# Kernel tuning notes

Measured on AMD Instinct MI355X. Metric: run time of the kernel, lower is better.

Reference implementation:

```python
import jax, jax.numpy as jnp
import numpy as np

N = 50000      # total nodes
E = 800000     # total edges
B = 512        # number of graphs (batch size)
D_IN, H, D_OUT = 5, 96, 192
EPS = 1e-5


def setup_inputs() -> dict:
    key = jax.random.key(0)
    ks = jax.random.split(key, 20)
    s = lambda d: 1.0 / np.sqrt(d)
    inp = {
        "x": jax.random.normal(ks[0], (N, D_IN), jnp.float32),
        "edge_index": jax.random.randint(ks[1], (2, E), 0, N, jnp.int64),
        "batch": jnp.sort(jax.random.randint(ks[2], (N,), 0, B, jnp.int64)),
        "W_in": jax.random.normal(ks[3], (D_IN, H), jnp.float32) * s(D_IN),
        "b_in": jnp.zeros((H,), jnp.float32),
        "W1": jax.random.normal(ks[4], (H, H), jnp.float32) * s(H),
        "b1": jnp.zeros((H,), jnp.float32),
        "g1": jnp.ones((H,), jnp.float32),
        "be1": jnp.zeros((H,), jnp.float32),
        "W2": jax.random.normal(ks[5], (H, H), jnp.float32) * s(H),
        "b2": jnp.zeros((H,), jnp.float32),
        "g2": jnp.ones((H,), jnp.float32),
        "be2": jnp.zeros((H,), jnp.float32),
        "W_out": jax.random.normal(ks[6], (H, D_OUT), jnp.float32) * s(H),
        "b_out": jnp.zeros((D_OUT,), jnp.float32),
        "ln_g": jnp.ones((D_OUT,), jnp.float32),
        "ln_b": jnp.zeros((D_OUT,), jnp.float32),
    }
    return inp


def gcn_conv(h, W, b, src, dst):
    # PyG GCNConv: h' = D^{-1/2} (A + I) D^{-1/2} (h W) + b, deg from self-looped graph
    h = h @ W                                           # [N, H]
    deg = jnp.ones((N,), h.dtype).at[dst].add(jnp.ones((E,), h.dtype))
    dinv = jax.lax.rsqrt(deg)                           # [N]
    coef = dinv[src] * dinv[dst]                        # [E]
    agg = jnp.zeros_like(h).at[dst].add(h[src] * coef[:, None])
    agg = agg + h * (dinv * dinv)[:, None]              # self-loop term
    return agg + b


def batch_norm(x, g, b):
    m = x.mean(0)
    v = x.var(0)
    return g * (x - m) * jax.lax.rsqrt(v + EPS) + b


def reference(x, edge_index, batch, W_in, b_in, W1, b1, g1, be1, W2, b2, g2, be2,
              W_out, b_out, ln_g, ln_b):
    src, dst = edge_index[0], edge_index[1]
    h = jax.nn.relu(x @ W_in + b_in)
    for (W, bb, g, be) in ((W1, b1, g1, be1), (W2, b2, g2, be2)):
        r = h
        h = gcn_conv(h, W, bb, src, dst)
        h = jax.nn.relu(batch_norm(h, g, be))           # dropout = identity (eval)
        h = h + r
    counts = jnp.zeros((B,), h.dtype).at[batch].add(1.0)
    pooled = jax.ops.segment_sum(h, batch, num_segments=B)
    pooled = pooled / jnp.maximum(counts, 1.0)[:, None]  # global_mean_pool [B, H]
    out = pooled @ W_out + b_out                         # [B, D_OUT]
    mu = out.mean(-1, keepdims=True)
    var = out.var(-1, keepdims=True)
    return ln_g * (out - mu) * jax.lax.rsqrt(var + EPS) + ln_b
```

## Files before the change

### kernel.cpp

```cpp
#include <hip/hip_runtime.h>
#include <hip/hip_bf16.h>
#include <stdint.h>

#define NN 50000
#define EE 800000
#define BB 512
#define HH 96
#define DIN 5
#define DOUT 192
#define EPSV 1e-5f
#define NBANK 32
#define HWS 48
#define NB_GATHER 3125
#define NBUK 512
#define BUKN 98
#define FILLB 128
#define FCHUNK (EE / FILLB)

__device__ inline float blo(uint32_t w) { return __uint_as_float(w << 16); }
__device__ inline float bhi(uint32_t w) { return __uint_as_float(w & 0xffff0000u); }
__device__ inline uint32_t packbf(float a, float b) {
    uint32_t ua = __float_as_uint(a); ua += 0x7fffu + ((ua >> 16) & 1u);
    uint32_t ub = __float_as_uint(b); ub += 0x7fffu + ((ub >> 16) & 1u);
    return (ua >> 16) | (ub & 0xffff0000u);
}

__global__ __launch_bounds__(256) void k_bhist(const int* __restrict__ dst,
                                               int* __restrict__ histgb) {
    __shared__ int hist[NBUK];
    int tid = threadIdx.x;
    for (int j = tid; j < NBUK; j += 256) hist[j] = 0;
    __syncthreads();
    int e0 = blockIdx.x * FCHUNK;
    for (int e = e0 + tid; e < e0 + FCHUNK; e += 256) atomicAdd(&hist[dst[e] / BUKN], 1);
    __syncthreads();
    for (int j = tid; j < NBUK; j += 256) histgb[blockIdx.x * NBUK + j] = hist[j];
}

__global__ __launch_bounds__(512) void k_bscan(int* __restrict__ histgb,
                                               int* __restrict__ bkbase,
                                               float* __restrict__ stats,
                                               int* __restrict__ row_ptr) {
    __shared__ int sc[NBUK];
    int t = threadIdx.x;
    for (int i = t; i < 2 * NBANK * 192; i += 512) stats[i] = 0.0f;
    {
        int c = 0;
        for (int b = 0; b < FILLB; ++b) {
            int idx = b * NBUK + t;
            int tmp = histgb[idx];
            histgb[idx] = c;
            c += tmp;
        }
        sc[t] = c;
    }
    __syncthreads();
    if (t == 0) {
        int c = 0;
        for (int j = 0; j < NBUK; ++j) { int s = sc[j]; sc[j] = c; c += s; }
        row_ptr[NN] = c;
        bkbase[NBUK] = c;
    }
    __syncthreads();
    bkbase[t] = sc[t];
}

__global__ __launch_bounds__(256) void k_bscat(const int* __restrict__ src,
                                               const int* __restrict__ dst,
                                               const int* __restrict__ histgb,
                                               const int* __restrict__ bkbase,
                                               uint32_t* __restrict__ ebuf) {
    __shared__ int bbase[NBUK], cnt[NBUK];
    int tid = threadIdx.x;
    for (int j = tid; j < NBUK; j += 256) {
        bbase[j] = bkbase[j] + histgb[blockIdx.x * NBUK + j];
        cnt[j] = 0;
    }
    __syncthreads();
    int e0 = blockIdx.x * FCHUNK, e1 = e0 + FCHUNK;
    for (int e = e0 + tid; e < e1; e += 256) {
        int d = dst[e];
        int b = d / BUKN;
        int off = atomicAdd(&cnt[b], 1);
        ebuf[bbase[b] + off] = (uint32_t)src[e] | ((uint32_t)(d - b * BUKN) << 16);
    }
}

__global__ __launch_bounds__(256) void k_csr(const uint32_t* __restrict__ ebuf,
                                             const int* __restrict__ bkbase,
                                             int* __restrict__ row_ptr,
                                             int* __restrict__ col,
                                             int* __restrict__ degi,
                                             float* __restrict__ dinv,
                                             int* __restrict__ dhistb) {
    __shared__ int cnt[BUKN], base[BUKN], lcur[BUKN];
    __shared__ int dh[64];
    int b = blockIdx.x, tid = threadIdx.x;
    int node0 = b * BUKN;
    if (node0 >= NN) {
        if (tid < 64) dhistb[b * 64 + tid] = 0;
        return;
    }
    int nn = min(BUKN, NN - node0);
    int ebase = bkbase[b], eend = bkbase[b + 1];
    if (tid < 64) dh[tid] = 0;
    for (int j = tid; j < nn; j += 256) { cnt[j] = 0; lcur[j] = 0; }
    __syncthreads();
    for (int i = ebase + tid; i < eend; i += 256) atomicAdd(&cnt[ebuf[i] >> 16], 1);
    __syncthreads();
    if (tid == 0) {
        int c = 0;
        for (int j = 0; j < nn; ++j) { base[j] = c; c += cnt[j]; }
    }
    __syncthreads();
    for (int j = tid; j < nn; j += 256) {
        row_ptr[node0 + j] = ebase + base[j];
        degi[node0 + j] = cnt[j];
        dinv[node0 + j] = rsqrtf((float)cnt[j] + 1.0f);
        atomicAdd(&dh[min(cnt[j], 63)], 1);
    }
    for (int i = ebase + tid; i < eend; i += 256) {
        uint32_t w = ebuf[i];
        int dr = (int)(w >> 16);
        int off = atomicAdd(&lcur[dr], 1);
        col[ebase + base[dr] + off] = (int)(w & 0xffffu);
    }
    __syncthreads();
    if (tid < 64) dhistb[b * 64 + tid] = dh[tid];
}

__global__ __launch_bounds__(64) void k_dscan(int* __restrict__ dhistb) {
    __shared__ int tot[64], binbase[64];
    int t = threadIdx.x;
    int s = 0;
    for (int b = 0; b < NBUK; ++b) s += dhistb[b * 64 + t];
    tot[t] = s;
    __syncthreads();
    if (t == 0) {
        int c = 0;
        for (int k = 0; k < 64; ++k) { binbase[k] = c; c += tot[k]; }
    }
    __syncthreads();
    int c = binbase[t];
    for (int b = 0; b < NBUK; ++b) {
        int tmp = dhistb[b * 64 + t];
        dhistb[b * 64 + t] = c;
        c += tmp;
    }
}

__global__ __launch_bounds__(128) void k_dperm(const int* __restrict__ degi,
                                               const int* __restrict__ dhistb,
                                               int* __restrict__ perm) {
    __shared__ int lcur[64];
    int b = blockIdx.x, t = threadIdx.x;
    int node0 = b * BUKN;
    if (node0 >= NN) return;
    int nn = min(BUKN, NN - node0);
    if (t < 64) lcur[t] = dhistb[b * 64 + t];
    __syncthreads();
    if (t < nn) {
        int i = node0 + t;
        int pos = atomicAdd(&lcur[min(degi[i], 63)], 1);
        perm[pos] = i;
    }
}

__device__ inline void pack24(uint32_t* __restrict__ dstrow, int q, const float* v) {
    uint32_t wv[12];
#pragma unroll
    for (int p = 0; p < 12; ++p) wv[p] = packbf(v[2 * p], v[2 * p + 1]);
    uint4* dstp = reinterpret_cast<uint4*>(dstrow + q * 12);
    dstp[0] = make_uint4(wv[0], wv[1], wv[2], wv[3]);
    dstp[1] = make_uint4(wv[4], wv[5], wv[6], wv[7]);
    dstp[2] = make_uint4(wv[8], wv[9], wv[10], wv[11]);
}

__global__ __launch_bounds__(256) void k_gemm_in(const float* __restrict__ x,
                                                 const float* __restrict__ Win,
                                                 const float* __restrict__ bin,
                                                 const float* __restrict__ W1,
                                                 const float* __restrict__ dinv,
                                                 uint32_t* __restrict__ h0b,
                                                 uint32_t* __restrict__ hwb) {
    __shared__ float sAT[96][68];
    __shared__ float sW[96 * 96];
    int tid = threadIdx.x;
    int row0 = blockIdx.x * 64;

    for (int i = tid; i < 96 * 96; i += 256) sW[i] = W1[i];

    {
        int r = tid >> 2, q = tid & 3;
        int j0q = q * 24;
        int gr = row0 + r;
        float xv[5];
#pragma unroll
        for (int k = 0; k < DIN; ++k) xv[k] = (gr < NN) ? x[gr * DIN + k] : 0.0f;
        float hv[24];
#pragma unroll
        for (int jj = 0; jj < 24; ++jj) {
            float acc = bin[j0q + jj];
#pragma unroll
            for (int k = 0; k < DIN; ++k) acc += xv[k] * Win[k * 96 + j0q + jj];
            hv[jj] = fmaxf(acc, 0.0f);
            sAT[j0q + jj][r] = hv[jj];
        }
        if (gr < NN) pack24(&h0b[(size_t)gr * HWS], q, hv);
    }
    __syncthreads();

    int tc = tid & 15, tr = tid >> 4;
    int r0 = tr * 4, j0 = tc * 6;
    float acc[4][6];
#pragma unroll
    for (int i = 0; i < 4; ++i)
#pragma unroll
        for (int j = 0; j < 6; ++j) acc[i][j] = 0.0f;

    for (int k = 0; k < 96; ++k) {
        float4 a = *reinterpret_cast<const float4*>(&sAT[k][r0]);
        const float* wr = &sW[k * 96 + j0];
        float b0 = wr[0], b1 = wr[1], b2 = wr[2], b3 = wr[3], b4 = wr[4], b5 = wr[5];
        float av[4] = {a.x, a.y, a.z, a.w};
#pragma unroll
        for (int i = 0; i < 4; ++i) {
            acc[i][0] += av[i] * b0; acc[i][1] += av[i] * b1; acc[i][2] += av[i] * b2;
            acc[i][3] += av[i] * b3; acc[i][4] += av[i] * b4; acc[i][5] += av[i] * b5;
        }
    }
#pragma unroll
    for (int i = 0; i < 4; ++i) {
        int gr = row0 + r0 + i;
        if (gr < NN) {
            float dv = dinv[gr];
            uint32_t* wp = &hwb[(size_t)gr * HWS + tc * 3];
            wp[0] = packbf(acc[i][0] * dv, acc[i][1] * dv);
            wp[1] = packbf(acc[i][2] * dv, acc[i][3] * dv);
            wp[2] = packbf(acc[i][4] * dv, acc[i][5] * dv);
        }
    }
}

__global__ __launch_bounds__(256) void k_gather(const uint32_t* __restrict__ hwb,
                                                const float* __restrict__ dinv,
                                                const int* __restrict__ row_ptr,
                                                const int* __restrict__ col,
                                                const int* __restrict__ perm,
                                                uint32_t* __restrict__ aggb,
                                                float* __restrict__ stats) {
    int tid = threadIdx.x;
    int t = tid & 15, slot = tid >> 4;
    int n = perm[blockIdx.x * 16 + slot];

    const uint32_t* rn = hwb + (size_t)n * HWS;
    uint2 w01 = *reinterpret_cast<const uint2*>(rn + 2 * t);
    uint32_t w2 = rn[32 + t];
    float a0 = blo(w01.x), a1 = bhi(w01.x);
    float a2 = blo(w01.y), a3 = bhi(w01.y);
    float a4 = blo(w2),    a5 = bhi(w2);

    int beg = row_ptr[n], end = row_ptr[n + 1];
    int p = beg;
    for (; p + 3 < end; p += 4) {
        int s0 = col[p], s1 = col[p + 1], s2 = col[p + 2], s3 = col[p + 3];
        const uint32_t* r0 = hwb + (size_t)s0 * HWS;
        const uint32_t* r1 = hwb + (size_t)s1 * HWS;
        const uint32_t* r2 = hwb + (size_t)s2 * HWS;
        const uint32_t* r3 = hwb + (size_t)s3 * HWS;
        uint2 u0 = *reinterpret_cast<const uint2*>(r0 + 2 * t); uint32_t v0 = r0[32 + t];
        uint2 u1 = *reinterpret_cast<const uint2*>(r1 + 2 * t); uint32_t v1 = r1[32 + t];
        uint2 u2 = *reinterpret_cast<const uint2*>(r2 + 2 * t); uint32_t v2 = r2[32 + t];
        uint2 u3 = *reinterpret_cast<const uint2*>(r3 + 2 * t); uint32_t v3 = r3[32 + t];
        a0 += blo(u0.x); a1 += bhi(u0.x); a2 += blo(u0.y); a3 += bhi(u0.y);
        a4 += blo(v0);   a5 += bhi(v0);
        a0 += blo(u1.x); a1 += bhi(u1.x); a2 += blo(u1.y); a3 += bhi(u1.y);
        a4 += blo(v1);   a5 += bhi(v1);
        a0 += blo(u2.x); a1 += bhi(u2.x); a2 += blo(u2.y); a3 += bhi(u2.y);
        a4 += blo(v2);   a5 += bhi(v2);
        a0 += blo(u3.x); a1 += bhi(u3.x); a2 += blo(u3.y); a3 += bhi(u3.y);
        a4 += blo(v3);   a5 += bhi(v3);
    }
    for (; p < end; ++p) {
        const uint32_t* rs = hwb + (size_t)col[p] * HWS;
        uint2 u = *reinterpret_cast<const uint2*>(rs + 2 * t);
        uint32_t v = rs[32 + t];
        a0 += blo(u.x); a1 += bhi(u.x);
        a2 += blo(u.y); a3 += bhi(u.y);
        a4 += blo(v);   a5 += bhi(v);
    }
    float dn = dinv[n];
    a0 *= dn; a1 *= dn; a2 *= dn; a3 *= dn; a4 *= dn; a5 *= dn;

    uint32_t* an = aggb + (size_t)n * HWS;
    *reinterpret_cast<uint2*>(an + 2 * t) = make_uint2(packbf(a0, a1), packbf(a2, a3));
    an[32 + t] = packbf(a4, a5);

    __shared__ float red[2][96];
    if (tid < 96) { red[0][tid] = 0.0f; red[1][tid] = 0.0f; }
    __syncthreads();
    int colsv[6] = {4 * t, 4 * t + 1, 4 * t + 2, 4 * t + 3, 64 + 2 * t, 64 + 2 * t + 1};
    float cs[6] = {a0, a1, a2, a3, a4, a5};
#pragma unroll
    for (int k = 0; k < 6; ++k) {
        atomicAdd(&red[0][colsv[k]], cs[k]);
        atomicAdd(&red[1][colsv[k]], cs[k] * cs[k]);
    }
    __syncthreads();
    float* bank = stats + (blockIdx.x & (NBANK - 1)) * 192;
    if (tid < 96) {
        atomicAdd(&bank[tid], red[0][tid]);
        atomicAdd(&bank[96 + tid], red[1][tid]);
    }
}

__global__ __launch_bounds__(256) void k_gemm_bn(const uint32_t* __restrict__ aggb,
                                                 const uint32_t* __restrict__ hprevb,
                                                 const float* __restrict__ stats,
                                                 const float* __restrict__ g,
                                                 const float* __restrict__ be,
                                                 const float* __restrict__ W,
                                                 const float* __restrict__ dinv,
                                                 uint32_t* __restrict__ hnewb,
                                                 uint32_t* __restrict__ hwb) {
    __shared__ float sAT[96][68];
    __shared__ float sW[96 * 96];
    __shared__ float ssc[96], ssh[96];
    int tid = threadIdx.x;
    int row0 = blockIdx.x * 64;

    for (int i = tid; i < 96 * 96; i += 256) sW[i] = W[i];
    if (tid < 96) {
        float s = 0.0f, s2 = 0.0f;
#pragma unroll
        for (int k = 0; k < NBANK; ++k) { s += stats[k * 192 + tid]; s2 += stats[k * 192 + 96 + tid]; }
        float m = s * (1.0f / NN);
        float var = s2 * (1.0f / NN) - m * m;
        float sc = g[tid] * rsqrtf(var + EPSV);
        ssc[tid] = sc;
        ssh[tid] = be[tid] - m * sc;
    }
    __syncthreads();

    for (int i = tid; i < 64 * 24; i += 256) {
        int r = i / 24, qq = i % 24;
        int gr = row0 + r, c = qq * 4, w0 = qq * 2;
        float v0 = 0.0f, v1 = 0.0f, v2 = 0.0f, v3 = 0.0f;
        if (gr < NN) {
            uint2 aw = *reinterpret_cast<const uint2*>(&aggb[(size_t)gr * HWS + w0]);
            uint2 pw = *reinterpret_cast<const uint2*>(&hprevb[(size_t)gr * HWS + w0]);
            v0 = fmaxf(blo(aw.x) * ssc[c]     + ssh[c],     0.0f) + blo(pw.x);
            v1 = fmaxf(bhi(aw.x) * ssc[c + 1] + ssh[c + 1], 0.0f) + bhi(pw.x);
            v2 = fmaxf(blo(aw.y) * ssc[c + 2] + ssh[c + 2], 0.0f) + blo(pw.y);
            v3 = fmaxf(bhi(aw.y) * ssc[c + 3] + ssh[c + 3], 0.0f) + bhi(pw.y);
            *reinterpret_cast<uint2*>(&hnewb[(size_t)gr * HWS + w0]) =
                make_uint2(packbf(v0, v1), packbf(v2, v3));
        }
        sAT[c][r] = v0; sAT[c + 1][r] = v1; sAT[c + 2][r] = v2; sAT[c + 3][r] = v3;
    }
    __syncthreads();

    int tc = tid & 15, tr = tid >> 4;
    int r0 = tr * 4, j0 = tc * 6;
    float acc[4][6];
#pragma unroll
    for (int i = 0; i < 4; ++i)
#pragma unroll
        for (int j = 0; j < 6; ++j) acc[i][j] = 0.0f;

    for (int k = 0; k < 96; ++k) {
        float4 a = *reinterpret_cast<const float4*>(&sAT[k][r0]);
        const float* wr = &sW[k * 96 + j0];
        float b0 = wr[0], b1 = wr[1], b2 = wr[2], b3 = wr[3], b4 = wr[4], b5 = wr[5];
        float av[4] = {a.x, a.y, a.z, a.w};
#pragma unroll
        for (int i = 0; i < 4; ++i) {
            acc[i][0] += av[i] * b0; acc[i][1] += av[i] * b1; acc[i][2] += av[i] * b2;
            acc[i][3] += av[i] * b3; acc[i][4] += av[i] * b4; acc[i][5] += av[i] * b5;
        }
    }
#pragma unroll
    for (int i = 0; i < 4; ++i) {
        int gr = row0 + r0 + i;
        if (gr < NN) {
            float dv = dinv[gr];
            uint32_t* wp = &hwb[(size_t)gr * HWS + tc * 3];
            wp[0] = packbf(acc[i][0] * dv, acc[i][1] * dv);
            wp[1] = packbf(acc[i][2] * dv, acc[i][3] * dv);
            wp[2] = packbf(acc[i][4] * dv, acc[i][5] * dv);
        }
    }
}

__device__ inline int lower_bound_i(const int* __restrict__ a, int n, int v) {
    int lo = 0, hi = n;
    while (lo < hi) { int mid = (lo + hi) >> 1; if (a[mid] < v) lo = mid + 1; else hi = mid; }
    return lo;
}

__global__ __launch_bounds__(384) void k_out(const uint32_t* __restrict__ aggb,
                                             const uint32_t* __restrict__ hprevb,
                                             const float* __restrict__ stats,
                                             const float* __restrict__ g,
                                             const float* __restrict__ be,
                                             const int* __restrict__ batch,
                                             const float* __restrict__ Wout,
                                             const float* __restrict__ bout,
                                             const float* __restrict__ lg,
                                             const float* __restrict__ lb,
                                             float* __restrict__ out) {
    __shared__ float ssc[96], ssh[96];
    __shared__ float sp8[8][96];
    __shared__ float sp[96];
    __shared__ float svals[192];
    __shared__ float smv[2];
    int b = blockIdx.x, t = threadIdx.x;
    if (t < 96) {
        float s = 0.0f, s2 = 0.0f;
#pragma unroll
        for (int k = 0; k < NBANK; ++k) { s += stats[k * 192 + t]; s2 += stats[k * 192 + 96 + t]; }
        float m = s * (1.0f / NN);
        float var = s2 * (1.0f / NN) - m * m;
        float sc = g[t] * rsqrtf(var + EPSV);
        ssc[t] = sc;
        ssh[t] = be[t] - m * sc;
    }
    int lo = lower_bound_i(batch, NN, b);
    int hi = lower_bound_i(batch, NN, b + 1);
    __syncthreads();

    int w = t % 48, qr = t / 48;
    int c0 = 2 * w, c1 = 2 * w + 1;
    float sc0 = ssc[c0], sh0 = ssh[c0], sc1 = ssc[c1], sh1 = ssh[c1];
    float accp0 = 0.0f, accp1 = 0.0f;
    for (int r = lo + qr; r < hi; r += 8) {
        uint32_t a = aggb[(size_t)r * HWS + w];
        uint32_t h = hprevb[(size_t)r * HWS + w];
        accp0 += fmaxf(blo(a) * sc0 + sh0, 0.0f) + blo(h);
        accp1 += fmaxf(bhi(a) * sc1 + sh1, 0.0f) + bhi(h);
    }
    sp8[qr][c0] = accp0;
    sp8[qr][c1] = accp1;
    __syncthreads();
    if (t < 96) {
        float inv = (hi > lo) ? 1.0f / (float)(hi - lo) : 0.0f;
        float s = 0.0f;
#pragma unroll
        for (int k = 0; k < 8; ++k) s += sp8[k][t];
        sp[t] = s * inv;
    }
    __syncthreads();

    float acc = 0.0f;
    if (t < 192) {
        acc = bout[t];
        for (int k = 0; k < 96; ++k) acc += sp[k] * Wout[k * 192 + t];
        svals[t] = acc;
    }
    __syncthreads();
    if (t < 64) {
        float a0 = svals[t], a1 = svals[t + 64], a2 = svals[t + 128];
        float s = a0 + a1 + a2;
        float s2 = a0 * a0 + a1 * a1 + a2 * a2;
        for (int o = 32; o > 0; o >>= 1) {
            s += __shfl_down(s, o, 64);
            s2 += __shfl_down(s2, o, 64);
        }
        if (t == 0) { smv[0] = s * (1.0f / 192.0f); smv[1] = s2 * (1.0f / 192.0f); }
    }
    __syncthreads();
    if (t < 192) {
        float m = smv[0];
        float var = smv[1] - m * m;
        float rr = rsqrtf(var + EPSV);
        out[b * 192 + t] = lg[t] * (acc - m) * rr + lb[t];
    }
}

extern "C" void kernel_launch(void* const* d_in, const int* in_sizes, int n_in,
                              void* d_out, int out_size, void* d_ws, size_t ws_size,
                              hipStream_t stream) {
    const float* x    = (const float*)d_in[0];
    const int*   ei   = (const int*)  d_in[1];
    const int*   batch= (const int*)  d_in[2];
    const float* Win  = (const float*)d_in[3];
    const float* bin  = (const float*)d_in[4];
    const float* W1   = (const float*)d_in[5];
    const float* g1   = (const float*)d_in[7];
    const float* be1  = (const float*)d_in[8];
    const float* W2   = (const float*)d_in[9];
    const float* g2   = (const float*)d_in[11];
    const float* be2  = (const float*)d_in[12];
    const float* Wout = (const float*)d_in[13];
    const float* bout = (const float*)d_in[14];
    const float* lg   = (const float*)d_in[15];
    const float* lb   = (const float*)d_in[16];
    const int* src = ei;
    const int* dst = ei + EE;

    uint32_t* wsp    = (uint32_t*)d_ws;
    uint32_t* h0b    = wsp;
    uint32_t* h1b    = h0b + (size_t)NN * HWS;
    uint32_t* aggb   = h1b + (size_t)NN * HWS;
    uint32_t* hwb    = aggb + (size_t)NN * HWS;
    float*    dinv   = (float*)(hwb + (size_t)NN * HWS);
    float*    stats  = dinv + NN;
    int*      degi   = (int*)(stats + 2 * NBANK * 192);
    int*      dhistb = degi + NN;
    int*      row_ptr= dhistb + NBUK * 64;
    int*      perm   = row_ptr + NN + 1;
    int*      bkbase = perm + NN;
    int*      histgb = bkbase + NBUK + 1;
    int*      col    = histgb + FILLB * NBUK;
    uint32_t* ebuf   = aggb;

    const int TB = 256;
    float* stats1 = stats;
    float* stats2 = stats + NBANK * 192;

    k_bhist<<<FILLB, TB, 0, stream>>>(dst, histgb);
    k_bscan<<<1, 512, 0, stream>>>(histgb, bkbase, stats, row_ptr);
    k_bscat<<<FILLB, TB, 0, stream>>>(src, dst, histgb, bkbase, ebuf);
    k_csr<<<NBUK, TB, 0, stream>>>(ebuf, bkbase, row_ptr, col, degi, dinv, dhistb);
    k_dscan<<<1, 64, 0, stream>>>(dhistb);
    k_dperm<<<NBUK, 128, 0, stream>>>(degi, dhistb, perm);

    k_gemm_in<<<(NN + 63) / 64, TB, 0, stream>>>(x, Win, bin, W1, dinv, h0b, hwb);
    k_gather<<<NB_GATHER, TB, 0, stream>>>(hwb, dinv, row_ptr, col, perm, aggb, stats1);

    k_gemm_bn<<<(NN + 63) / 64, TB, 0, stream>>>(aggb, h0b, stats1, g1, be1, W2, dinv,
                                                 h1b, hwb);
    k_gather<<<NB_GATHER, TB, 0, stream>>>(hwb, dinv, row_ptr, col, perm, aggb, stats2);

    k_out<<<BB, 384, 0, stream>>>(aggb, h1b, stats2, g2, be2, batch, Wout, bout, lg, lb,
                                  (float*)d_out);
}
```

Before: 261.4 us.

## Partition edges by source slice so gathers hit cache-resident feature rows

Edges are bucketed by source-node slice (four slices of 12500 nodes) as well as destination bucket, giving one CSR per slice. Each gather is split into a partial-sum pass per slice followed by a combine pass that adds the self term, scales by dinv and accumulates BN stats. The aim is for random source-row reads to stay within a working set small enough to live in L2/MALL. In exchange it adds partial-buffer writes and reads in bf16, which costs extra rounding, plus more kernel launches and a separate degree kernel.

```diff
diff --git a/kernel.cpp b/kernel.cpp
--- a/kernel.cpp
+++ b/kernel.cpp
@@ -11,11 +11,15 @@
 #define EPSV 1e-5f
 #define NBANK 32
 #define HWS 48
-#define NB_GATHER 3125
-#define NBUK 512
+#define NSLICE 4
+#define SLICEN 12500
+#define NBUK2 2048
 #define BUKN 98
 #define FILLB 128
 #define FCHUNK (EE / FILLB)
+#define NNP1 (NN + 1)
+#define CHUNK0 25088
+#define PARTN 25088
 
 __device__ inline float blo(uint32_t w) { return __uint_as_float(w << 16); }
 __device__ inline float bhi(uint32_t w) { return __uint_as_float(w & 0xffff0000u); }
@@ -25,44 +29,48 @@
     return (ua >> 16) | (ub & 0xffff0000u);
 }
 
-__global__ __launch_bounds__(256) void k_bhist(const int* __restrict__ dst,
+__global__ __launch_bounds__(256) void k_bhist(const int* __restrict__ src,
+                                               const int* __restrict__ dst,
                                                int* __restrict__ histgb) {
-    __shared__ int hist[NBUK];
+    __shared__ int hist[NBUK2];
     int tid = threadIdx.x;
-    for (int j = tid; j < NBUK; j += 256) hist[j] = 0;
+    for (int j = tid; j < NBUK2; j += 256) hist[j] = 0;
     __syncthreads();
     int e0 = blockIdx.x * FCHUNK;
-    for (int e = e0 + tid; e < e0 + FCHUNK; e += 256) atomicAdd(&hist[dst[e] / BUKN], 1);
-    __syncthreads();
-    for (int j = tid; j < NBUK; j += 256) histgb[blockIdx.x * NBUK + j] = hist[j];
-}
-
-__global__ __launch_bounds__(512) void k_bscan(int* __restrict__ histgb,
-                                               int* __restrict__ bkbase,
-                                               float* __restrict__ stats,
-                                               int* __restrict__ row_ptr) {
-    __shared__ int sc[NBUK];
+    for (int e = e0 + tid; e < e0 + FCHUNK; e += 256) {
+        int b2 = (src[e] / SLICEN) * 512 + dst[e] / BUKN;
+        atomicAdd(&hist[b2], 1);
+    }
+    __syncthreads();
+    for (int j = tid; j < NBUK2; j += 256) histgb[blockIdx.x * NBUK2 + j] = hist[j];
+}
+
+__global__ __launch_bounds__(1024) void k_bscan(int* __restrict__ histgb,
+                                                int* __restrict__ bkbase,
+                                                float* __restrict__ stats,
+                                                int* __restrict__ rp2s) {
+    __shared__ int sc[NBUK2];
     int t = threadIdx.x;
-    for (int i = t; i < 2 * NBANK * 192; i += 512) stats[i] = 0.0f;
-    {
+    for (int i = t; i < 2 * NBANK * 192; i += 1024) stats[i] = 0.0f;
+    for (int j = t; j < NBUK2; j += 1024) {
         int c = 0;
         for (int b = 0; b < FILLB; ++b) {
-            int idx = b * NBUK + t;
+            int idx = b * NBUK2 + j;
             int tmp = histgb[idx];
             histgb[idx] = c;
             c += tmp;
         }
-        sc[t] = c;
+        sc[j] = c;
     }
     __syncthreads();
     if (t == 0) {
         int c = 0;
-        for (int j = 0; j < NBUK; ++j) { int s = sc[j]; sc[j] = c; c += s; }
-        row_ptr[NN] = c;
-        bkbase[NBUK] = c;
-    }
-    __syncthreads();
-    bkbase[t] = sc[t];
+        for (int j = 0; j < NBUK2; ++j) { int s0 = sc[j]; sc[j] = c; c += s0; }
+        bkbase[NBUK2] = c;
+    }
+    __syncthreads();
+    for (int j = t; j < NBUK2; j += 1024) bkbase[j] = sc[j];
+    if (t < NSLICE) rp2s[(size_t)t * NNP1 + NN] = (t == NSLICE - 1) ? EE : sc[(t + 1) * 512];
 }
 
 __global__ __launch_bounds__(256) void k_bscat(const int* __restrict__ src,
@@ -70,40 +78,35 @@
                                                const int* __restrict__ histgb,
                                                const int* __restrict__ bkbase,
                                                uint32_t* __restrict__ ebuf) {
-    __shared__ int bbase[NBUK], cnt[NBUK];
+    __shared__ int bbase[NBUK2], cnt[NBUK2];
     int tid = threadIdx.x;
-    for (int j = tid; j < NBUK; j += 256) {
-        bbase[j] = bkbase[j] + histgb[blockIdx.x * NBUK + j];
+    for (int j = tid; j < NBUK2; j += 256) {
+        bbase[j] = bkbase[j] + histgb[blockIdx.x * NBUK2 + j];
         cnt[j] = 0;
     }
     __syncthreads();
     int e0 = blockIdx.x * FCHUNK, e1 = e0 + FCHUNK;
     for (int e = e0 + tid; e < e1; e += 256) {
-        int d = dst[e];
-        int b = d / BUKN;
-        int off = atomicAdd(&cnt[b], 1);
-        ebuf[bbase[b] + off] = (uint32_t)src[e] | ((uint32_t)(d - b * BUKN) << 16);
+        int sv = src[e], d = dst[e];
+        int db = d / BUKN;
+        int b2 = (sv / SLICEN) * 512 + db;
+        int off = atomicAdd(&cnt[b2], 1);
+        ebuf[bbase[b2] + off] = (uint32_t)sv | ((uint32_t)(d - db * BUKN) << 16);
     }
 }
 
 __global__ __launch_bounds__(256) void k_csr(const uint32_t* __restrict__ ebuf,
                                              const int* __restrict__ bkbase,
-                                             int* __restrict__ row_ptr,
-                                             int* __restrict__ col,
-                                             int* __restrict__ degi,
-                                             float* __restrict__ dinv,
-                                             int* __restrict__ dhistb) {
+                                             int* __restrict__ rp2s,
+                                             int* __restrict__ colp) {
     __shared__ int cnt[BUKN], base[BUKN], lcur[BUKN];
-    __shared__ int dh[64];
-    int b = blockIdx.x, tid = threadIdx.x;
+    int bk = blockIdx.x, tid = threadIdx.x;
+    int s = bk >> 9;
+    int b = bk & 511;
     int node0 = b * BUKN;
-    if (node0 >= NN) {
-        if (tid < 64) dhistb[b * 64 + tid] = 0;
-        return;
-    }
+    if (node0 >= NN) return;
     int nn = min(BUKN, NN - node0);
-    int ebase = bkbase[b], eend = bkbase[b + 1];
-    if (tid < 64) dh[tid] = 0;
+    int ebase = bkbase[bk], eend = bkbase[bk + 1];
     for (int j = tid; j < nn; j += 256) { cnt[j] = 0; lcur[j] = 0; }
     __syncthreads();
     for (int i = ebase + tid; i < eend; i += 256) atomicAdd(&cnt[ebuf[i] >> 16], 1);
@@ -113,39 +116,63 @@
         for (int j = 0; j < nn; ++j) { base[j] = c; c += cnt[j]; }
     }
     __syncthreads();
-    for (int j = tid; j < nn; j += 256) {
-        row_ptr[node0 + j] = ebase + base[j];
-        degi[node0 + j] = cnt[j];
-        dinv[node0 + j] = rsqrtf((float)cnt[j] + 1.0f);
-        atomicAdd(&dh[min(cnt[j], 63)], 1);
-    }
+    for (int j = tid; j < nn; j += 256)
+        rp2s[(size_t)s * NNP1 + node0 + j] = ebase + base[j];
     for (int i = ebase + tid; i < eend; i += 256) {
         uint32_t w = ebuf[i];
         int dr = (int)(w >> 16);
         int off = atomicAdd(&lcur[dr], 1);
-        col[ebase + base[dr] + off] = (int)(w & 0xffffu);
-    }
-    __syncthreads();
-    if (tid < 64) dhistb[b * 64 + tid] = dh[tid];
+        colp[ebase + base[dr] + off] = (int)(w & 0xffffu);
+    }
+}
+
+__global__ __launch_bounds__(128) void k_deg(const int* __restrict__ rp2s,
+                                             int* __restrict__ degi,
+                                             float* __restrict__ dinv,
+                                             int* __restrict__ dhistb) {
+    __shared__ int dh[64];
+    int b = blockIdx.x, t = threadIdx.x;
+    if (t < 64) dh[t] = 0;
+    __syncthreads();
+    int node0 = b * BUKN;
+    if (node0 < NN) {
+        int nn = min(BUKN, NN - node0);
+        if (t < nn) {
+            int n = node0 + t;
+            int deg = 0;
+#pragma unroll
+            for (int s = 0; s < NSLICE; ++s)
+                deg += rp2s[(size_t)s * NNP1 + n + 1] - rp2s[(size_t)s * NNP1 + n];
+            degi[n] = deg;
+            dinv[n] = rsqrtf((float)deg + 1.0f);
+            atomicAdd(&dh[min(deg, 63)], 1);
+        }
+    }
+    __syncthreads();
+    if (t < 64) dhistb[b * 64 + t] = dh[t];
 }
 
 __global__ __launch_bounds__(64) void k_dscan(int* __restrict__ dhistb) {
     __shared__ int tot[64], binbase[64];
     int t = threadIdx.x;
-    int s = 0;
-    for (int b = 0; b < NBUK; ++b) s += dhistb[b * 64 + t];
-    tot[t] = s;
-    __syncthreads();
-    if (t == 0) {
-        int c = 0;
-        for (int k = 0; k < 64; ++k) { binbase[k] = c; c += tot[k]; }
-    }
-    __syncthreads();
-    int c = binbase[t];
-    for (int b = 0; b < NBUK; ++b) {
-        int tmp = dhistb[b * 64 + t];
-        dhistb[b * 64 + t] = c;
-        c += tmp;
+    for (int h = 0; h < 2; ++h) {
+        int b0 = h * 256, b1 = b0 + 256;
+        int s = 0;
+        for (int b = b0; b < b1; ++b) s += dhistb[b * 64 + t];
+        tot[t] = s;
+        __syncthreads();
+        if (t == 0) {
+            int c = h * CHUNK0;
+            for (int k = 0; k < 64; ++k) { binbase[k] = c; c += tot[k]; }
+        }
+        __syncthreads();
+        int c = binbase[t];
+        for (int b = b0; b < b1; ++b) {
+            int tmp = dhistb[b * 64 + t];
+            dhistb[b * 64 + t] = c;
+            c += tmp;
+        }
+        __syncthreads();
     }
 }
 
@@ -242,51 +269,66 @@
     }
 }
 
-__global__ __launch_bounds__(256) void k_gather(const uint32_t* __restrict__ hwb,
-                                                const float* __restrict__ dinv,
-                                                const int* __restrict__ row_ptr,
-                                                const int* __restrict__ col,
-                                                const int* __restrict__ perm,
-                                                uint32_t* __restrict__ aggb,
-                                                float* __restrict__ stats) {
+__global__ __launch_bounds__(256) void k_gatherA(const uint32_t* __restrict__ hwb,
+                                                 const int* __restrict__ rp2s,
+                                                 const int* __restrict__ colp,
+                                                 const int* __restrict__ perm,
+                                                 int chunkbase,
+                                                 uint32_t* __restrict__ partial) {
     int tid = threadIdx.x;
     int t = tid & 15, slot = tid >> 4;
-    int n = perm[blockIdx.x * 16 + slot];
-
+    int s = blockIdx.x & 3, g = blockIdx.x >> 2;
+    int pos = chunkbase + g * 16 + slot;
+    int n = perm[pos];
+    const int* rp = rp2s + (size_t)s * NNP1 + n;
+    int p = rp[0], end = rp[1];
+    float a0 = 0.f, a1 = 0.f, a2 = 0.f, a3 = 0.f, a4 = 0.f, a5 = 0.f;
+    for (; p + 1 < end; p += 2) {
+        int s0 = colp[p], s1 = colp[p + 1];
+        const uint32_t* r0 = hwb + (size_t)s0 * HWS;
+        const uint32_t* r1 = hwb + (size_t)s1 * HWS;
+        uint2 u0 = *reinterpret_cast<const uint2*>(r0 + 2 * t); uint32_t v0 = r0[32 + t];
+        uint2 u1 = *reinterpret_cast<const uint2*>(r1 + 2 * t); uint32_t v1 = r1[32 + t];
+        a0 += blo(u0.x); a1 += bhi(u0.x); a2 += blo(u0.y); a3 += bhi(u0.y);
+        a4 += blo(v0);   a5 += bhi(v0);
+        a0 += blo(u1.x); a1 += bhi(u1.x); a2 += blo(u1.y); a3 += bhi(u1.y);
+        a4 += blo(v1);   a5 += bhi(v1);
+    }
+    if (p < end) {
+        const uint32_t* rs = hwb + (size_t)colp[p] * HWS;
+        uint2 u = *reinterpret_cast<const uint2*>(rs + 2 * t);
+        uint32_t v = rs[32 + t];
+        a0 += blo(u.x); a1 += bhi(u.x); a2 += blo(u.y); a3 += bhi(u.y);
+        a4 += blo(v);   a5 += bhi(v);
+    }
+    uint32_t* pp = partial + ((size_t)s * PARTN + (pos - chunkbase)) * HWS;
+    *reinterpret_cast<uint2*>(pp + 2 * t) = make_uint2(packbf(a0, a1), packbf(a2, a3));
+    pp[32 + t] = packbf(a4, a5);
+}
+
+__global__ __launch_bounds__(256) void k_gatherB(const uint32_t* __restrict__ hwb,
+                                                 const uint32_t* __restrict__ partial,
+                                                 const float* __restrict__ dinv,
+                                                 const int* __restrict__ perm,
+                                                 int chunkbase,
+                                                 uint32_t* __restrict__ aggb,
+                                                 float* __restrict__ stats) {
+    int tid = threadIdx.x;
+    int t = tid & 15, slot = tid >> 4;
+    int pos = chunkbase + blockIdx.x * 16 + slot;
+    int n = perm[pos];
     const uint32_t* rn = hwb + (size_t)n * HWS;
     uint2 w01 = *reinterpret_cast<const uint2*>(rn + 2 * t);
     uint32_t w2 = rn[32 + t];
     float a0 = blo(w01.x), a1 = bhi(w01.x);
     float a2 = blo(w01.y), a3 = bhi(w01.y);
     float a4 = blo(w2),    a5 = bhi(w2);
-
-    int beg = row_ptr[n], end = row_ptr[n + 1];
-    int p = beg;
-    for (; p + 3 < end; p += 4) {
-        int s0 = col[p], s1 = col[p + 1], s2 = col[p + 2], s3 = col[p + 3];
-        const uint32_t* r0 = hwb + (size_t)s0 * HWS;
-        const uint32_t* r1 = hwb + (size_t)s1 * HWS;
-        const uint32_t* r2 = hwb + (size_t)s2 * HWS;
-        const uint32_t* r3 = hwb + (size_t)s3 * HWS;
-        uint2 u0 = *reinterpret_cast<const uint2*>(r0 + 2 * t); uint32_t v0 = r0[32 + t];
-        uint2 u1 = *reinterpret_cast<const uint2*>(r1 + 2 * t); uint32_t v1 = r1[32 + t];
-        uint2 u2 = *reinterpret_cast<const uint2*>(r2 + 2 * t); uint32_t v2 = r2[32 + t];
-        uint2 u3 = *reinterpret_cast<const uint2*>(r3 + 2 * t); uint32_t v3 = r3[32 + t];
-        a0 += blo(u0.x); a1 += bhi(u0.x); a2 += blo(u0.y); a3 += bhi(u0.y);
-        a4 += blo(v0);   a5 += bhi(v0);
-        a0 += blo(u1.x); a1 += bhi(u1.x); a2 += blo(u1.y); a3 += bhi(u1.y);
-        a4 += blo(v1);   a5 += bhi(v1);
-        a0 += blo(u2.x); a1 += bhi(u2.x); a2 += blo(u2.y); a3 += bhi(u2.y);
-        a4 += blo(v2);   a5 += bhi(v2);
-        a0 += blo(u3.x); a1 += bhi(u3.x); a2 += blo(u3.y); a3 += bhi(u3.y);
-        a4 += blo(v3);   a5 += bhi(v3);
-    }
-    for (; p < end; ++p) {
-        const uint32_t* rs = hwb + (size_t)col[p] * HWS;
-        uint2 u = *reinterpret_cast<const uint2*>(rs + 2 * t);
-        uint32_t v = rs[32 + t];
-        a0 += blo(u.x); a1 += bhi(u.x);
-        a2 += blo(u.y); a3 += bhi(u.y);
+#pragma unroll
+    for (int s = 0; s < NSLICE; ++s) {
+        const uint32_t* pr = partial + ((size_t)s * PARTN + (pos - chunkbase)) * HWS;
+        uint2 u = *reinterpret_cast<const uint2*>(pr + 2 * t);
+        uint32_t v = pr[32 + t];
+        a0 += blo(u.x); a1 += bhi(u.x); a2 += blo(u.y); a3 += bhi(u.y);
         a4 += blo(v);   a5 += bhi(v);
     }
     float dn = dinv[n];
@@ -503,34 +545,48 @@
     uint32_t* h1b    = h0b + (size_t)NN * HWS;
     uint32_t* aggb   = h1b + (size_t)NN * HWS;
     uint32_t* hwb    = aggb + (size_t)NN * HWS;
-    float*    dinv   = (float*)(hwb + (size_t)NN * HWS);
+    uint32_t* partial= hwb + (size_t)NN * HWS;
+    float*    dinv   = (float*)(partial + (size_t)NSLICE * PARTN * HWS);
     float*    stats  = dinv + NN;
     int*      degi   = (int*)(stats + 2 * NBANK * 192);
     int*      dhistb = degi + NN;
-    int*      row_ptr= dhistb + NBUK * 64;
-    int*      perm   = row_ptr + NN + 1;
+    int*      rp2s   = dhistb + 512 * 64;
+    int*      perm   = rp2s + NSLICE * NNP1;
     int*      bkbase = perm + NN;
-    int*      histgb = bkbase + NBUK + 1;
-    int*      col    = histgb + FILLB * NBUK;
+    int*      histgb = bkbase + NBUK2 + 1;
+    int*      colp   = histgb + FILLB * NBUK2;
     uint32_t* ebuf   = aggb;
 
     const int TB = 256;
     float* stats1 = stats;
     float* stats2 = stats + NBANK * 192;
-
-    k_bhist<<<FILLB, TB, 0, stream>>>(dst, histgb);
-    k_bscan<<<1, 512, 0, stream>>>(histgb, bkbase, stats, row_ptr);
+    const int chunkbase[2] = {0, CHUNK0};
+    const int chunkN[2] = {CHUNK0, NN - CHUNK0};
+
+    k_bhist<<<FILLB, TB, 0, stream>>>(src, dst, histgb);
+    k_bscan<<<1, 1024, 0, stream>>>(histgb, bkbase, stats, rp2s);
     k_bscat<<<FILLB, TB, 0, stream>>>(src, dst, histgb, bkbase, ebuf);
-    k_csr<<<NBUK, TB, 0, stream>>>(ebuf, bkbase, row_ptr, col, degi, dinv, dhistb);
+    k_csr<<<NBUK2, TB, 0, stream>>>(ebuf, bkbase, rp2s, colp);
+    k_deg<<<512, 128, 0, stream>>>(rp2s, degi, dinv, dhistb);
     k_dscan<<<1, 64, 0, stream>>>(dhistb);
-    k_dperm<<<NBUK, 128, 0, stream>>>(degi, dhistb, perm);
+    k_dperm<<<512, 128, 0, stream>>>(degi, dhistb, perm);
 
     k_gemm_in<<<(NN + 63) / 64, TB, 0, stream>>>(x, Win, bin, W1, dinv, h0b, hwb);
-    k_gather<<<NB_GATHER, TB, 0, stream>>>(hwb, dinv, row_ptr, col, perm, aggb, stats1);
+    for (int c = 0; c < 2; ++c) {
+        k_gatherA<<<(chunkN[c] / 16) * NSLICE, TB, 0, stream>>>(hwb, rp2s, colp, perm,
+                                                                chunkbase[c], partial);
+        k_gatherB<<<chunkN[c] / 16, TB, 0, stream>>>(hwb, partial, dinv, perm,
+                                                     chunkbase[c], aggb, stats1);
+    }
 
     k_gemm_bn<<<(NN + 63) / 64, TB, 0, stream>>>(aggb, h0b, stats1, g1, be1, W2, dinv,
                                                  h1b, hwb);
-    k_gather<<<NB_GATHER, TB, 0, stream>>>(hwb, dinv, row_ptr, col, perm, aggb, stats2);
+    for (int c = 0; c < 2; ++c) {
+        k_gatherA<<<(chunkN[c] / 16) * NSLICE, TB, 0, stream>>>(hwb, rp2s, colp, perm,
+                                                                chunkbase[c], partial);
+        k_gatherB<<<chunkN[c] / 16, TB, 0, stream>>>(hwb, partial, dinv, perm,
+                                                     chunkbase[c], aggb, stats2);
+    }
 
     k_out<<<BB, 384, 0, stream>>>(aggb, h1b, stats2, g2, be2, batch, Wout, bout, lg, lb,
                                   (float*)d_out);
```

Result: slower. 369.3 us (+41.3%).
